# Optimization experiments

Measured on AMD Instinct MI355X. Metric: run time of the kernel, lower is better.

Reference implementation:

```python
import jax, jax.numpy as jnp
import numpy as np

LN_EPS = 1e-5
B, T, H = 32, 1024, 1024


def _layer_norm(v, g, b):
    m = v.mean(-1, keepdims=True)
    var = ((v - m) ** 2).mean(-1, keepdims=True)
    return (v - m) / jnp.sqrt(var + LN_EPS) * g + b


def setup_inputs() -> dict:
    key = jax.random.key(0)
    ks = jax.random.split(key, 10)
    s_t = 1.0 / np.sqrt(T)
    s_h = 1.0 / np.sqrt(H)
    return {
        "x": jax.random.normal(ks[0], (B, T, H), jnp.float32),
        # temporal MLP (square T x T, triangular-masked), torch Linear layout [out, in]
        "tw1": jax.random.uniform(ks[1], (T, T), jnp.float32, -s_t, s_t),
        "tb1": jax.random.uniform(ks[2], (T,), jnp.float32, -s_t, s_t),
        "tw2": jax.random.uniform(ks[3], (T, T), jnp.float32, -s_t, s_t),
        "tb2": jax.random.uniform(ks[4], (T,), jnp.float32, -s_t, s_t),
        # channel MLP (square H x H)
        "cw1": jax.random.uniform(ks[5], (H, H), jnp.float32, -s_h, s_h),
        "cb1": jax.random.uniform(ks[6], (H,), jnp.float32, -s_h, s_h),
        "cw2": jax.random.uniform(ks[7], (H, H), jnp.float32, -s_h, s_h),
        "cb2": jax.random.uniform(ks[8], (H,), jnp.float32, -s_h, s_h),
        # LayerNorm affine params
        "ln1_g": jnp.ones((H,), jnp.float32),
        "ln1_b": jnp.zeros((H,), jnp.float32),
        "ln2_g": jnp.ones((H,), jnp.float32),
        "ln2_b": jnp.zeros((H,), jnp.float32),
    }


def reference(x, tw1, tb1, tw2, tb2, cw1, cb1, cw2, cb2, ln1_g, ln1_b, ln2_g, ln2_b):
    t = tw1.shape[0]
    mask = jnp.tril(jnp.ones((t, t), x.dtype))  # diagonal=0: include self
    # temporal mixing: LN -> swap -> masked Linear -> GELU -> masked Linear -> swap
    y = _layer_norm(x, ln1_g, ln1_b)
    y = jnp.swapaxes(y, 1, 2)  # [B, H, T]
    y = y @ (mask * tw1).T + tb1
    y = jax.nn.gelu(y, approximate=False)
    y = y @ (mask * tw2).T + tb2
    y = jnp.swapaxes(y, 1, 2)  # [B, T, H]
    x = x + y
    # channel mixing: LN -> Linear -> GELU -> Linear
    y2 = _layer_norm(x, ln2_g, ln2_b)
    y2 = jax.nn.gelu(y2 @ cw1.T + cb1, approximate=False) @ cw2.T + cb2
    return x + y2
```

## Files before the change

### kernel.cpp

```cpp
#include <hip/hip_runtime.h>
#include <hip/hip_bf16.h>

#define BDIM 32
#define TDIM 1024
#define HDIM 1024
#define AS1 __attribute__((address_space(1)))
#define AS3 __attribute__((address_space(3)))

typedef __attribute__((ext_vector_type(8))) short short8;
typedef __attribute__((ext_vector_type(8))) unsigned short ushort8;
typedef __attribute__((ext_vector_type(4))) unsigned short u16x4;
typedef __attribute__((ext_vector_type(4))) float f32x4;

__device__ __forceinline__ float b2f(unsigned short h){ return __uint_as_float(((unsigned)h)<<16); }
__device__ __forceinline__ unsigned short f2b(float f){
  unsigned u = __float_as_uint(f);
  u += 0x7fffu + ((u>>16)&1u);
  return (unsigned short)(u>>16);
}
__device__ __forceinline__ float gelu_f(float v){ return 0.5f*v*(1.0f+erff(v*0.70710678118f)); }
__device__ __forceinline__ void stv(float* p, float v){ *p = v; }
__device__ __forceinline__ void stv(unsigned short* p, float v){ *p = f2b(v); }
__device__ __forceinline__ float ldr(float v){ return v; }
__device__ __forceinline__ float ldr(unsigned short v){ return b2f(v); }

__global__ void prep_weights(const float* __restrict__ w1, const float* __restrict__ w2,
                             const float* __restrict__ c1, const float* __restrict__ c2,
                             unsigned short* __restrict__ w1m, unsigned short* __restrict__ w2m,
                             unsigned short* __restrict__ c1b, unsigned short* __restrict__ c2b){
  int idx = blockIdx.x*blockDim.x + threadIdx.x;
  int e = idx*4;
  int i = e >> 10, j0 = e & 1023;
  f32x4 a = *(const f32x4*)(w1+e);
  f32x4 b = *(const f32x4*)(w2+e);
  f32x4 c = *(const f32x4*)(c1+e);
  f32x4 d = *(const f32x4*)(c2+e);
  u16x4 av, bv, cv, dv;
  #pragma unroll
  for (int q=0;q<4;++q){
    float am = (j0+q <= i) ? a[q] : 0.f;
    float bm = (j0+q <= i) ? b[q] : 0.f;
    av[q]=f2b(am); bv[q]=f2b(bm); cv[q]=f2b(c[q]); dv[q]=f2b(d[q]);
  }
  *(u16x4*)(w1m+e)=av; *(u16x4*)(w2m+e)=bv; *(u16x4*)(c1b+e)=cv; *(u16x4*)(c2b+e)=dv;
}

__global__ void ln_stats(const float* __restrict__ p, float* __restrict__ mean,
                         float* __restrict__ rstd){
  int wid = threadIdx.x>>6, lane = threadIdx.x&63;
  int row = blockIdx.x*4 + wid;
  const float* pr = p + (size_t)row*HDIM;
  float s=0.f, s2=0.f;
  #pragma unroll
  for (int it=0; it<4; ++it){
    f32x4 v = *(const f32x4*)(pr + it*256 + lane*4);
    #pragma unroll
    for (int c=0;c<4;++c){ s += v[c]; s2 += v[c]*v[c]; }
  }
  #pragma unroll
  for (int off=32; off>0; off>>=1){ s += __shfl_xor(s,off,64); s2 += __shfl_xor(s2,off,64); }
  if (lane==0){
    float m = s * (1.0f/HDIM);
    float var = s2 * (1.0f/HDIM) - m*m;
    mean[row]=m; rstd[row]=rsqrtf(var + 1e-5f);
  }
}

__global__ void ln_norm_transpose(const float* __restrict__ x, const float* __restrict__ mean,
                                  const float* __restrict__ rstd, const float* __restrict__ g,
                                  const float* __restrict__ bta, unsigned short* __restrict__ xnT){
  __shared__ float tile[64][65];
  int t0 = blockIdx.x*64, h0 = blockIdx.y*64, b = blockIdx.z;
  int tid = threadIdx.x;
  int rr = tid>>3, c8 = tid&7;
  size_t base = (size_t)b*TDIM*HDIM;
  #pragma unroll
  for (int p=0;p<2;++p){
    int r = rr + p*32;
    int trow = t0 + r;
    float m = mean[b*TDIM + trow], rs = rstd[b*TDIM + trow];
    f32x4 v0 = *(const f32x4*)(x + base + (size_t)trow*HDIM + h0 + c8*8);
    f32x4 v1 = *(const f32x4*)(x + base + (size_t)trow*HDIM + h0 + c8*8 + 4);
    #pragma unroll
    for (int c=0;c<4;++c){
      int h = c8*8+c;
      tile[r][h]   = (v0[c]-m)*rs*g[h0+h]   + bta[h0+h];
      tile[r][h+4] = (v1[c]-m)*rs*g[h0+h+4] + bta[h0+h+4];
    }
  }
  __syncthreads();
  #pragma unroll
  for (int p=0;p<2;++p){
    int hr = rr + p*32;
    ushort8 ov;
    #pragma unroll
    for (int c=0;c<8;++c) ov[c] = f2b(tile[c8*8+c][hr]);
    *(ushort8*)(xnT + base + (size_t)(h0+hr)*TDIM + t0 + c8*8) = ov;
  }
}

__global__ void ln_fused(const unsigned short* __restrict__ p, const float* __restrict__ g,
                         const float* __restrict__ bta, unsigned short* __restrict__ o){
  int wid = threadIdx.x>>6, lane = threadIdx.x&63;
  size_t row = (size_t)blockIdx.x*4 + wid;
  const unsigned short* pr = p + row*HDIM + lane*16;
  ushort8 v0 = *(const ushort8*)(pr);
  ushort8 v1 = *(const ushort8*)(pr+8);
  float f[16];
  float s=0.f, s2=0.f;
  #pragma unroll
  for (int c=0;c<8;++c){ f[c]=b2f(v0[c]); f[c+8]=b2f(v1[c]); }
  #pragma unroll
  for (int c=0;c<16;++c){ s += f[c]; s2 += f[c]*f[c]; }
  #pragma unroll
  for (int off=32; off>0; off>>=1){ s += __shfl_xor(s,off,64); s2 += __shfl_xor(s2,off,64); }
  float m = s * (1.0f/HDIM);
  float rs = rsqrtf(s2*(1.0f/HDIM) - m*m + 1e-5f);
  int h0 = lane*16;
  ushort8 o0, o1;
  #pragma unroll
  for (int c=0;c<8;++c){
    o0[c] = f2b((f[c]-m)*rs*g[h0+c] + bta[h0+c]);
    o1[c] = f2b((f[c+8]-m)*rs*g[h0+c+8] + bta[h0+c+8]);
  }
  *(ushort8*)(o + row*HDIM + h0) = o0;
  *(ushort8*)(o + row*HDIM + h0 + 8) = o1;
}

#define GATE(N) asm volatile("s_waitcnt vmcnt(" #N ")" ::: "memory")
#define BAR()   __builtin_amdgcn_s_barrier()

template<int MODE, typename CT, typename RT>
__global__ __launch_bounds__(512,1)
void gemmq(const unsigned short* __restrict__ act, const unsigned short* __restrict__ wgt,
           CT* __restrict__ C, const float* __restrict__ bias, const RT* __restrict__ resid){
  extern __shared__ char LDS[];
  const int bid = blockIdx.x;
  int panel, inner;
  if constexpr (MODE==1 || MODE==2){
    inner = 3 - (bid >> 7);
    int lb = bid & 127;
    panel = (lb & 7)*16 + (lb >> 3);
  } else {
    int tile = (bid & 7)*64 + (bid >> 3);
    panel = tile >> 2;
    inner = tile & 3;
  }
  const unsigned short *pa, *pb;
  size_t cbase; int rg0, cg0, kend;
  if constexpr (MODE==1){
    int b = panel>>2, mt = panel&3;
    pa = act + (size_t)b*1048576 + (size_t)mt*262144;
    pb = wgt + (size_t)inner*262144;
    kend = (inner+1)*256;
    cbase = (size_t)b*1048576; rg0 = mt*256; cg0 = inner*256;
  } else if constexpr (MODE==2){
    int b = panel>>2, nt = panel&3;
    pa = wgt + (size_t)inner*262144;
    pb = act + (size_t)b*1048576 + (size_t)nt*262144;
    kend = (inner+1)*256;
    cbase = (size_t)b*1048576; rg0 = inner*256; cg0 = nt*256;
  } else {
    pa = act + (size_t)panel*262144;
    pb = wgt + (size_t)inner*262144;
    kend = 1024;
    cbase = 0; rg0 = panel*256; cg0 = inner*256;
  }
  const int tid = threadIdx.x, lane = tid&63, wid = tid>>6;
  const int wrow = (wid>>2)*64;
  const int wcol = (wid&3)*32;
  const int l15 = lane&15, l4b = (lane>>4)<<4;
  f32x4 acc[8][4];
  #pragma unroll
  for (int i=0;i<8;++i)
    #pragma unroll
    for (int j=0;j<4;++j) acc[i][j] = (f32x4)(0.f);

  const int NT = kend>>6;

  auto STAGE = [&](int dt, int half, int st){
    const unsigned short* src = (half<2) ? pa : pb;
    const int rbase = (half&1)<<7;
    char* dst = LDS + ((dt&1)<<16) + (half<<14);
    const int k0 = st<<6;
    #pragma unroll
    for (int l=0;l<2;++l){
      int W = tid*16 + (l<<13);
      int r = W>>7;
      int cs = (W&127) ^ ((r&7)<<4);
      __builtin_amdgcn_global_load_lds(
        (const AS1 void*)(src + (size_t)(rbase+r)*1024 + k0 + (cs>>1)),
        (AS3 void*)(dst + W), 16, 0, 0);
    }
  };
  auto STG = [&](int tt, int half, int t_now){ STAGE(tt, half, tt<NT ? tt : t_now); };

  auto LDA = [&](int buf, int qa, int i, int s)->short8{
    int ra = wrow + i*16 + l15;
    int L = (ra<<7) + (((s<<6) + l4b) ^ ((ra&7)<<4));
    return *(const short8*)(LDS + (buf<<16) + (qa<<14) + L);
  };
  auto LDB = [&](int buf, int qb, int j, int s)->short8{
    int rb = wcol + j*16 + l15;
    int L = (rb<<7) + (((s<<6) + l4b) ^ ((rb&7)<<4));
    return *(const short8*)(LDS + (buf<<16) + ((2+qb)<<14) + L);
  };

  short8 aR[2][4], bR[2][2];

#define MFMAQ(qa,qb)                                                         \
  __builtin_amdgcn_s_setprio(1);                                             \
  _Pragma("unroll") for (int s=0;s<2;++s)                                    \
    _Pragma("unroll") for (int i=0;i<4;++i)                                  \
      _Pragma("unroll") for (int j=0;j<2;++j)                                \
        acc[(qa)*4+i][(qb)*2+j] = __builtin_amdgcn_mfma_f32_16x16x32_bf16(   \
            aR[s][i], bR[s][j], acc[(qa)*4+i][(qb)*2+j], 0,0,0);             \
  __builtin_amdgcn_s_setprio(0);

  STAGE(0,0,0); STAGE(0,2,0); STAGE(0,1,0); STAGE(0,3,0);
  STAGE(1,0, 1<NT ? 1 : 0);
  GATE(6); BAR();

  for (int t=0; t<NT; ++t){
    const int buf = t&1;
    #pragma unroll
    for (int s=0;s<2;++s){
      #pragma unroll
      for (int i=0;i<4;++i) aR[s][i] = LDA(buf,0,i,s);
      #pragma unroll
      for (int j=0;j<2;++j) bR[s][j] = LDB(buf,0,j,s);
    }
    STG(t+1, 2, t);
    GATE(4); BAR();
    MFMAQ(0,0)
    #pragma unroll
    for (int s=0;s<2;++s)
      #pragma unroll
      for (int j=0;j<2;++j) bR[s][j] = LDB(buf,1,j,s);
    STG(t+1, 1, t);
    MFMAQ(0,1)
    BAR();
    #pragma unroll
    for (int s=0;s<2;++s)
      #pragma unroll
      for (int i=0;i<4;++i) aR[s][i] = LDA(buf,1,i,s);
    STG(t+1, 3, t);
    MFMAQ(1,1)
    #pragma unroll
    for (int s=0;s<2;++s)
      #pragma unroll
      for (int j=0;j<2;++j) bR[s][j] = LDB(buf,0,j,s);
    STG(t+2, 0, t);
    MFMAQ(1,0)
    BAR();
  }
#undef MFMAQ

  #pragma unroll
  for (int I=0;I<8;++I){
    int rbase = rg0 + (I>>2)*128 + wrow + (I&3)*16 + ((lane>>4)<<2);
    #pragma unroll
    for (int J=0;J<4;++J){
      int cg = cg0 + (J>>1)*128 + wcol + (J&1)*16 + l15;
      float bn = (MODE!=2) ? bias[cg] : 0.f;
      #pragma unroll
      for (int r=0;r<4;++r){
        int rg = rbase + r;
        float v = acc[I][J][r];
        if (MODE==1 || MODE==3){ v += bn; v = gelu_f(v); }
        else if (MODE==2){ v += bias[rg]; v += ldr(resid[cbase + (size_t)rg*1024 + cg]); }
        else { v += bn; v += ldr(resid[cbase + (size_t)rg*1024 + cg]); }
        stv(&C[cbase + (size_t)rg*1024 + cg], v);
      }
    }
  }
}

extern "C" void kernel_launch(void* const* d_in, const int* in_sizes, int n_in,
                              void* d_out, int out_size, void* d_ws, size_t ws_size,
                              hipStream_t stream){
  const float* x    = (const float*)d_in[0];
  const float* tw1  = (const float*)d_in[1];
  const float* tb1  = (const float*)d_in[2];
  const float* tw2  = (const float*)d_in[3];
  const float* tb2  = (const float*)d_in[4];
  const float* cw1  = (const float*)d_in[5];
  const float* cb1  = (const float*)d_in[6];
  const float* cw2  = (const float*)d_in[7];
  const float* cb2  = (const float*)d_in[8];
  const float* g1   = (const float*)d_in[9];
  const float* bb1  = (const float*)d_in[10];
  const float* g2   = (const float*)d_in[11];
  const float* bb2  = (const float*)d_in[12];
  float* out = (float*)d_out;

  char* ws = (char*)d_ws;
  unsigned short* bufA = (unsigned short*)(ws);
  unsigned short* bufB = (unsigned short*)(ws + 67108864);
  unsigned short* xmid = (unsigned short*)(ws + 134217728);
  unsigned short* w1m  = (unsigned short*)(ws + 201326592);
  unsigned short* w2m  = (unsigned short*)(ws + 203423744);
  unsigned short* c1b  = (unsigned short*)(ws + 205520896);
  unsigned short* c2b  = (unsigned short*)(ws + 207618048);
  float* meanb = (float*)(ws + 209715200);
  float* rstdb = (float*)(ws + 209846272);

  prep_weights<<<1024,256,0,stream>>>(tw1,tw2,cw1,cw2,w1m,w2m,c1b,c2b);
  ln_stats<<<8192,256,0,stream>>>(x, meanb, rstdb);
  ln_norm_transpose<<<dim3(16,16,32),256,0,stream>>>(x, meanb, rstdb, g1, bb1, bufA);
  gemmq<1,unsigned short,float><<<512,512,131072,stream>>>(bufA, w1m, bufB, tb1, (const float*)nullptr);
  gemmq<2,unsigned short,float><<<512,512,131072,stream>>>(bufB, w2m, xmid, tb2, x);
  ln_fused<<<8192,256,0,stream>>>(xmid, g2, bb2, bufA);
  gemmq<3,unsigned short,unsigned short><<<512,512,131072,stream>>>(bufA, c1b, bufB, cb1, (const unsigned short*)nullptr);
  gemmq<4,float,unsigned short><<<512,512,131072,stream>>>(bufB, c2b, out, cb2, xmid);
}
```

Measured before the change: 451.3 us.

## Use smaller 128x128 tile GEMM kernel for channel MLP layers

Adds a new GEMM kernel with 128x128 output tiles, 256 threads, 64KB LDS double buffering and two blocks per CU, and uses it for the two channel-MLP GEMMs instead of the large-tile 512-thread kernel. Smaller tiles give more blocks (2048) and better occupancy and load balance, and the block-index swizzle groups tiles that share the same activation panel. In exchange, operand reuse per tile is lower, so more global and LDS traffic is needed per FLOP.

```diff
diff --git a/kernel.cpp b/kernel.cpp
--- a/kernel.cpp
+++ b/kernel.cpp
@@ -276,6 +276,98 @@
   }
 }
 
+template<int MODE, typename CT, typename RT>
+__global__ __launch_bounds__(256,2)
+void gemms(const unsigned short* __restrict__ act, const unsigned short* __restrict__ wgt,
+           CT* __restrict__ C, const float* __restrict__ bias, const RT* __restrict__ resid){
+  extern __shared__ char LDS[];
+  const int bid = blockIdx.x;
+  const int tile = (bid & 7)*256 + (bid >> 3);
+  const int panel = tile >> 3;
+  const int inner = tile & 7;
+  const unsigned short* pa = act + (size_t)panel*131072;
+  const unsigned short* pb = wgt + (size_t)inner*131072;
+  const int rg0 = panel*128, cg0 = inner*128;
+  const int NT = 16;
+  const int tid = threadIdx.x, lane = tid&63, wid = tid>>6;
+  const int wrow = (wid>>1)*64;
+  const int wcol = (wid&1)*64;
+  const int l15 = lane&15, l4b = (lane>>4)<<4;
+  f32x4 acc[4][4];
+  #pragma unroll
+  for (int i=0;i<4;++i)
+    #pragma unroll
+    for (int j=0;j<4;++j) acc[i][j] = (f32x4)(0.f);
+
+  auto STAGE = [&](int buf, int op, int st){
+    const unsigned short* src = op ? pb : pa;
+    char* dst = LDS + buf*32768 + op*16384;
+    const int k0 = st<<6;
+    #pragma unroll
+    for (int l=0;l<4;++l){
+      int W = tid*16 + (l<<12);
+      int r = W>>7;
+      int cs = (W&127) ^ ((r&7)<<4);
+      __builtin_amdgcn_global_load_lds(
+        (const AS1 void*)(src + (size_t)r*1024 + k0 + (cs>>1)),
+        (AS3 void*)(dst + W), 16, 0, 0);
+    }
+  };
+  auto LDA = [&](int buf, int i, int s)->short8{
+    int ra = wrow + i*16 + l15;
+    int L = (ra<<7) + (((s<<6) + l4b) ^ ((ra&7)<<4));
+    return *(const short8*)(LDS + buf*32768 + L);
+  };
+  auto LDB = [&](int buf, int j, int s)->short8{
+    int rb = wcol + j*16 + l15;
+    int L = (rb<<7) + (((s<<6) + l4b) ^ ((rb&7)<<4));
+    return *(const short8*)(LDS + buf*32768 + 16384 + L);
+  };
+
+  STAGE(0,0,0); STAGE(0,1,0);
+  GATE(0); BAR();
+
+  for (int t=0; t<NT; ++t){
+    const int buf = t&1;
+    const int nsrc = (t+1 < NT) ? t+1 : t;
+    STAGE(buf^1, 0, nsrc); STAGE(buf^1, 1, nsrc);
+    #pragma unroll
+    for (int s=0;s<2;++s){
+      short8 aR[4];
+      #pragma unroll
+      for (int i=0;i<4;++i) aR[i] = LDA(buf,i,s);
+      #pragma unroll
+      for (int j=0;j<4;++j){
+        short8 bv = LDB(buf,j,s);
+        __builtin_amdgcn_s_setprio(1);
+        #pragma unroll
+        for (int i=0;i<4;++i)
+          acc[i][j] = __builtin_amdgcn_mfma_f32_16x16x32_bf16(aR[i], bv, acc[i][j], 0,0,0);
+        __builtin_amdgcn_s_setprio(0);
+      }
+    }
+    GATE(0); BAR();
+  }
+
+  #pragma unroll
+  for (int i=0;i<4;++i){
+    int rbase = rg0 + wrow + i*16 + ((lane>>4)<<2);
+    #pragma unroll
+    for (int j=0;j<4;++j){
+      int cg = cg0 + wcol + j*16 + l15;
+      float bn = bias[cg];
+      #pragma unroll
+      for (int r=0;r<4;++r){
+        int rg = rbase + r;
+        float v = acc[i][j][r];
+        if (MODE==3){ v += bn; v = gelu_f(v); }
+        else { v += bn; v += ldr(resid[(size_t)rg*1024 + cg]); }
+        stv(&C[(size_t)rg*1024 + cg], v);
+      }
+    }
+  }
+}
+
 extern "C" void kernel_launch(void* const* d_in, const int* in_sizes, int n_in,
                               void* d_out, int out_size, void* d_ws, size_t ws_size,
                               hipStream_t stream){
@@ -311,6 +403,6 @@
   gemmq<1,unsigned short,float><<<512,512,131072,stream>>>(bufA, w1m, bufB, tb1, (const float*)nullptr);
   gemmq<2,unsigned short,float><<<512,512,131072,stream>>>(bufB, w2m, xmid, tb2, x);
   ln_fused<<<8192,256,0,stream>>>(xmid, g2, bb2, bufA);
-  gemmq<3,unsigned short,unsigned short><<<512,512,131072,stream>>>(bufA, c1b, bufB, cb1, (const unsigned short*)nullptr);
-  gemmq<4,float,unsigned short><<<512,512,131072,stream>>>(bufB, c2b, out, cb2, xmid);
-}
+  gemms<3,unsigned short,unsigned short><<<2048,256,65536,stream>>>(bufA, c1b, bufB, cb1, (const unsigned short*)nullptr);
+  gemms<4,float,unsigned short><<<2048,256,65536,stream>>>(bufB, c2b, out, cb2, xmid);
+}
```

Result: slower. 463.2 us (+2.6%).
